# Kernel optimization log

Measured on AMD Instinct MI355X. Metric: run time of the kernel, lower is better.

## Reference

```python
import jax, jax.numpy as jnp
import numpy as np

B, N, D, HEADS, P, C = 64, 197, 768, 12, 12, 200
ARC_S, ARC_M = 30.0, 0.5


def layer_norm(x, g, b, eps=1e-5):
    m = jnp.mean(x, axis=-1, keepdims=True)
    v = jnp.var(x, axis=-1, keepdims=True)
    return (x - m) / jnp.sqrt(v + eps) * g + b


def setup_inputs() -> dict:
    key = jax.random.key(0)
    ks = jax.random.split(key, 16)
    sc = 0.02
    return {
        'hidden': jax.random.normal(ks[0], (B, N, D), jnp.float32),
        'attns': jax.random.uniform(ks[1], (4, B, HEADS, N, N), jnp.float32),
        'labels': jax.random.randint(ks[2], (B,), 0, C),
        'ln1_g': jnp.ones((D,), jnp.float32),
        'ln1_b': jnp.zeros((D,), jnp.float32),
        'w_in': jax.random.normal(ks[3], (3 * D, D), jnp.float32) * sc,
        'b_in': jnp.zeros((3 * D,), jnp.float32),
        'w_out': jax.random.normal(ks[4], (D, D), jnp.float32) * sc,
        'b_out': jnp.zeros((D,), jnp.float32),
        'ln2_g': jnp.ones((D,), jnp.float32),
        'ln2_b': jnp.zeros((D,), jnp.float32),
        'w_pool': jax.random.normal(ks[5], (1, D), jnp.float32) * sc,
        'b_pool': jnp.zeros((1,), jnp.float32),
        'pool_temp': jnp.float32(1.0),
        'w_mlp': jax.random.normal(ks[6], (D, D), jnp.float32) * sc,
        'b_mlp': jnp.zeros((D,), jnp.float32),
        'arc_w': jax.random.normal(ks[7], (C, 2 * D), jnp.float32) * sc,
    }


def reference(hidden, attns, labels, ln1_g, ln1_b, w_in, b_in, w_out, b_out,
              ln2_g, ln2_b, w_pool, b_pool, pool_temp, w_mlp, b_mlp, arc_w):
    cls_embed = hidden[:, 0]              # [B, D]
    patch_embeds = hidden[:, 1:]          # [B, N-1, D]

    # Multi-layer attention fusion: mean over heads, CLS row, drop CLS col.
    attn_scores = attns.mean(axis=2)[:, :, 0, 1:].mean(axis=0)  # [B, N-1]

    # Top-k part selection + gather.
    idx = jax.lax.top_k(attn_scores, P)[1]                       # [B, P]
    parts = jnp.take_along_axis(patch_embeds, idx[:, :, None], axis=1)  # [B,P,D]
    parts = layer_norm(parts, ln1_g, ln1_b)

    # Multi-head self-attention over parts (eval mode, no dropout).
    hd = D // HEADS
    qkv = parts @ w_in.T + b_in                                  # [B,P,3D]
    q, k, v = jnp.split(qkv, 3, axis=-1)
    def heads(t):
        return t.reshape(B, P, HEADS, hd).transpose(0, 2, 1, 3)  # [B,H,P,hd]
    q, k, v = heads(q), heads(k), heads(v)
    scores = jnp.einsum('bhqd,bhkd->bhqk', q, k) / jnp.sqrt(jnp.float32(hd))
    a = jax.nn.softmax(scores, axis=-1)
    o = jnp.einsum('bhqk,bhkd->bhqd', a, v)
    o = o.transpose(0, 2, 1, 3).reshape(B, P, D)
    attn_out = o @ w_out.T + b_out
    attn_out = layer_norm(attn_out, ln2_g, ln2_b)

    # Temperature-softmax weighted pooling.
    raw_w = (attn_out @ w_pool.T + b_pool)[..., 0]               # [B,P]
    weights = jax.nn.softmax(raw_w / jnp.maximum(pool_temp, 0.3), axis=1)
    part_feat = jnp.sum(attn_out * weights[..., None], axis=1)   # [B,D]
    part_feat = jax.nn.relu(part_feat @ w_mlp.T + b_mlp)

    fusion = jnp.concatenate([cls_embed, part_feat], axis=1)     # [B,2D]

    # ArcFace margin (train logits with labels).
    fn = fusion / jnp.linalg.norm(fusion, axis=-1, keepdims=True)
    wn = arc_w / jnp.linalg.norm(arc_w, axis=-1, keepdims=True)
    cosine = fn @ wn.T                                           # [B,C]
    sine = jnp.sqrt(jnp.clip(1.0 - cosine ** 2, 0.0, 1.0))
    cos_m, sin_m = np.cos(ARC_M), np.sin(ARC_M)
    th = np.cos(np.pi - ARC_M)
    mm = np.sin(np.pi - ARC_M) * ARC_M
    phi = cosine * cos_m - sine * sin_m
    phi = jnp.where(cosine > th, phi, cosine - mm)
    one_hot = jax.nn.one_hot(labels, C, dtype=cosine.dtype)
    logits = (one_hot * phi + (1.0 - one_hot) * cosine) * ARC_S
    return logits
```

## Files before the change

kernel.cpp:

```cpp
#include <hip/hip_runtime.h>
#include <hip/hip_bf16.h>
#include <float.h>
#include <math.h>

#define BB 64
#define NNtok 197
#define DD 768
#define HH 12
#define PP 12
#define CC 200
#define NPATCH 196

typedef short bf16x8 __attribute__((ext_vector_type(8)));
typedef float f32x4 __attribute__((ext_vector_type(4)));

__device__ __forceinline__ unsigned short bf16_bits(float x) {
  __hip_bfloat16 h = __float2bfloat16(x);
  return *reinterpret_cast<unsigned short*>(&h);
}
__device__ __forceinline__ float u2f(unsigned int u) {
  union { unsigned int u; float f; } cv; cv.u = u; return cv.f;
}
__device__ __forceinline__ float bfu(unsigned short us) {
  union { unsigned int u; float f; } cv; cv.u = ((unsigned int)us) << 16; return cv.f;
}

__global__ __launch_bounds__(256) void k1_front(
    const float* __restrict__ hidden, const float* __restrict__ attns,
    const float* __restrict__ g, const float* __restrict__ be,
    const float* __restrict__ w1, const float* __restrict__ w2,
    const float* __restrict__ w3, __hip_bfloat16* __restrict__ o1,
    __hip_bfloat16* __restrict__ o2, __hip_bfloat16* __restrict__ o3,
    __hip_bfloat16* __restrict__ parts) {
  int t = threadIdx.x, bi = blockIdx.x;
  if (bi >= 64) {
    for (int i = (bi - 64) * 256 + t; i < 737280; i += 256 * 256) {
      const float* src; __hip_bfloat16* dst; int off;
      if (i < 442368) { src = w1; dst = o1; off = i; }
      else if (i < 589824) { src = w2; dst = o2; off = i - 442368; }
      else { src = w3; dst = o3; off = i - 589824; }
      float4 v = ((const float4*)src)[off];
      union { unsigned short u[4]; ushort4 v4; } p;
      p.u[0] = bf16_bits(v.x); p.u[1] = bf16_bits(v.y);
      p.u[2] = bf16_bits(v.z); p.u[3] = bf16_bits(v.w);
      ((ushort4*)dst)[off] = p.v4;
    }
    return;
  }
  int b = bi;
  __shared__ float sc[256];
  __shared__ int sel_s[PP];
  int wv = t >> 6, ln = t & 63;
  float acc = -FLT_MAX;
  if (t < NPATCH) {
    acc = 0.f;
#pragma unroll
    for (int l = 0; l < 4; l++) {
      float part = 0.f;
#pragma unroll
      for (int h = 0; h < HH; h++) {
        size_t base = (size_t)((l * BB + b) * HH + h) * ((size_t)NNtok * NNtok);
        part += attns[base + 1 + t];
      }
      acc += part * (1.f / 12.f);
    }
    acc *= 0.25f;
  }
  sc[t] = acc;
  __syncthreads();
  if (t < 64) {
    float v[4]; int idx[4];
#pragma unroll
    for (int j = 0; j < 4; j++) { idx[j] = t + j * 64; v[j] = sc[idx[j]]; }
    for (int it = 0; it < PP; ++it) {
      float bv = v[0]; int bidx = idx[0];
#pragma unroll
      for (int j = 1; j < 4; j++)
        if (v[j] > bv || (v[j] == bv && idx[j] < bidx)) { bv = v[j]; bidx = idx[j]; }
      float cv = bv; int ci = bidx;
#pragma unroll
      for (int off = 32; off > 0; off >>= 1) {
        float ov = __shfl_xor(cv, off); int oi = __shfl_xor(ci, off);
        if (ov > cv || (ov == cv && oi < ci)) { cv = ov; ci = oi; }
      }
      if (t == 0) sel_s[it] = ci;
#pragma unroll
      for (int j = 0; j < 4; j++)
        if (idx[j] == ci) v[j] = -FLT_MAX;
    }
  }
  __syncthreads();
#pragma unroll
  for (int q = 0; q < 3; q++) {
    int i = wv * 3 + q;
    const float* row = hidden + ((size_t)b * NNtok + 1 + sel_s[i]) * DD;
    float x[12], s1 = 0.f, s2 = 0.f;
#pragma unroll
    for (int k = 0; k < 12; k++) {
      x[k] = row[ln + 64 * k];
      s1 += x[k]; s2 += x[k] * x[k];
    }
#pragma unroll
    for (int off = 32; off > 0; off >>= 1) {
      s1 += __shfl_xor(s1, off); s2 += __shfl_xor(s2, off);
    }
    float m = s1 * (1.f / DD);
    float rstd = rsqrtf(s2 * (1.f / DD) - m * m + 1e-5f);
    __hip_bfloat16* outp_ = parts + ((size_t)b * PP + i) * DD;
#pragma unroll
    for (int k = 0; k < 12; k++) {
      int d = ln + 64 * k;
      outp_[d] = __float2bfloat16((x[k] - m) * rstd * g[d] + be[d]);
    }
  }
}

__global__ __launch_bounds__(256) void k2_mid(
    const __hip_bfloat16* __restrict__ parts, const __hip_bfloat16* __restrict__ w_in_bf,
    const float* __restrict__ b_in, const __hip_bfloat16* __restrict__ w_out_bf,
    float* __restrict__ part_ws) {
  int bi = blockIdx.x;
  int b = bi >> 2, hg = bi & 3;
  int t = threadIdx.x;
  int wave = t >> 6, lane = t & 63, lr = lane & 15, kg = lane >> 4;
  __shared__ __align__(16) unsigned short qkv3[3][16][192];
  __shared__ __align__(16) unsigned short o3[16][192];
  __shared__ float scores[432];

  int pr = lr < 12 ? lr : 11;
  const __hip_bfloat16* Ab = parts + ((size_t)b * 12 + pr) * DD + kg * 8;
  int wrow[9];
#pragma unroll
  for (int nf = 0; nf < 9; nf++) {
    int lc = wave * 144 + nf * 16 + lr;
    int s = lc / 192, d2 = lc - s * 192;
    wrow[nf] = s * 768 + hg * 192 + d2;
  }
  f32x4 acc[9];
#pragma unroll
  for (int nf = 0; nf < 9; nf++) { acc[nf][0]=0.f; acc[nf][1]=0.f; acc[nf][2]=0.f; acc[nf][3]=0.f; }
  for (int k0 = 0; k0 < 768; k0 += 32) {
    bf16x8 af = *(const bf16x8*)(Ab + k0);
    bf16x8 wf[9];
#pragma unroll
    for (int nf = 0; nf < 9; nf++)
      wf[nf] = *(const bf16x8*)(w_in_bf + (size_t)wrow[nf] * DD + kg * 8 + k0);
#pragma unroll
    for (int nf = 0; nf < 9; nf++)
      acc[nf] = __builtin_amdgcn_mfma_f32_16x16x32_bf16(af, wf[nf], acc[nf], 0, 0, 0);
  }
#pragma unroll
  for (int nf = 0; nf < 9; nf++) {
    int lc = wave * 144 + nf * 16 + lr;
    int s = lc / 192, d2 = lc - s * 192;
    float bv = b_in[s * 768 + hg * 192 + d2];
#pragma unroll
    for (int r = 0; r < 4; r++) {
      int p = kg * 4 + r;
      qkv3[s][p][d2] = bf16_bits(acc[nf][r] + bv);
    }
  }
  __syncthreads();

  for (int e = t; e < 432; e += 256) {
    int h = e / 144, rem = e - h * 144;
    int i = rem / 12, j = rem - i * 12;
    float s = 0.f;
#pragma unroll
    for (int d = 0; d < 64; d++)
      s += bfu(qkv3[0][i][h * 64 + d]) * bfu(qkv3[1][j][h * 64 + d]);
    scores[e] = s * 0.125f;
  }
  __syncthreads();
  if (t < 36) {
    int h = t / 12, i = t - h * 12;
    float* row = scores + h * 144 + i * 12;
    float m = -FLT_MAX;
#pragma unroll
    for (int j = 0; j < 12; j++) m = fmaxf(m, row[j]);
    float e2[12], sum = 0.f;
#pragma unroll
    for (int j = 0; j < 12; j++) { e2[j] = expf(row[j] - m); sum += e2[j]; }
    float inv = 1.f / sum;
#pragma unroll
    for (int j = 0; j < 12; j++) row[j] = e2[j] * inv;
  }
  __syncthreads();
  for (int o = t; o < 2304; o += 256) {
    int i = o / 192, d2 = o - i * 192;
    int h = d2 >> 6;
    float s = 0.f;
#pragma unroll
    for (int j = 0; j < 12; j++)
      s += scores[h * 144 + i * 12 + j] * bfu(qkv3[2][j][d2]);
    o3[i][d2] = bf16_bits(s);
  }
  __syncthreads();

  f32x4 acc2[12];
#pragma unroll
  for (int jf = 0; jf < 12; jf++) { acc2[jf][0]=0.f; acc2[jf][1]=0.f; acc2[jf][2]=0.f; acc2[jf][3]=0.f; }
  const unsigned short* Ob = &o3[0][0] + lr * 192 + kg * 8;
  for (int k0 = 0; k0 < 192; k0 += 32) {
    bf16x8 af = *(const bf16x8*)(Ob + k0);
    bf16x8 wf[12];
#pragma unroll
    for (int jf = 0; jf < 12; jf++) {
      int j = wave * 192 + jf * 16 + lr;
      wf[jf] = *(const bf16x8*)(w_out_bf + (size_t)j * DD + hg * 192 + kg * 8 + k0);
    }
#pragma unroll
    for (int jf = 0; jf < 12; jf++)
      acc2[jf] = __builtin_amdgcn_mfma_f32_16x16x32_bf16(af, wf[jf], acc2[jf], 0, 0, 0);
  }
#pragma unroll
  for (int jf = 0; jf < 12; jf++) {
    int j = wave * 192 + jf * 16 + lr;
#pragma unroll
    for (int r = 0; r < 4; r++) {
      int p = kg * 4 + r;
      if (p < 12)
        part_ws[(((size_t)b * 4 + hg) * 12 + p) * DD + j] = acc2[jf][r];
    }
  }
}

__global__ __launch_bounds__(256) void k3_back(
    const float* __restrict__ part_ws, const float* __restrict__ b_out,
    const float* __restrict__ g, const float* __restrict__ be,
    const float* __restrict__ wp, const float* __restrict__ bp,
    const float* __restrict__ ptemp, const __hip_bfloat16* __restrict__ wmlp,
    const float* __restrict__ bmlp, float* __restrict__ pmlp) {
  int bi = blockIdx.x;
  int b = bi >> 2, q4 = bi & 3;
  int t = threadIdx.x, wv = t >> 6, ln = t & 63;
  __shared__ float a12[12 * 768];
  __shared__ float raww_s[12];
  __shared__ float pfeat[768];
  for (int u = t; u < 9216; u += 256) {
    int j = u % 768;
    float s = b_out[j];
#pragma unroll
    for (int hg = 0; hg < 4; hg++)
      s += part_ws[(((size_t)b * 4 + hg) * 12) * DD + u];
    a12[u] = s;
  }
  __syncthreads();
#pragma unroll
  for (int q = 0; q < 3; q++) {
    int r = wv * 3 + q;
    float x[12], s1 = 0.f, s2 = 0.f;
#pragma unroll
    for (int k = 0; k < 12; k++) {
      x[k] = a12[r * 768 + ln + 64 * k];
      s1 += x[k]; s2 += x[k] * x[k];
    }
#pragma unroll
    for (int off = 32; off > 0; off >>= 1) {
      s1 += __shfl_xor(s1, off); s2 += __shfl_xor(s2, off);
    }
    float m = s1 * (1.f / DD);
    float rstd = rsqrtf(s2 * (1.f / DD) - m * m + 1e-5f);
    float pl = 0.f;
#pragma unroll
    for (int k = 0; k < 12; k++) {
      int d = ln + 64 * k;
      float y = (x[k] - m) * rstd * g[d] + be[d];
      a12[r * 768 + d] = y;
      pl += y * wp[d];
    }
#pragma unroll
    for (int off = 32; off > 0; off >>= 1) pl += __shfl_xor(pl, off);
    if (ln == 0) raww_s[r] = pl + bp[0];
  }
  __syncthreads();
  float wts[12];
  {
    float inv = 1.f / fmaxf(ptemp[0], 0.3f);
    float z[12], mx = -FLT_MAX;
#pragma unroll
    for (int p = 0; p < 12; p++) { z[p] = raww_s[p] * inv; mx = fmaxf(mx, z[p]); }
    float s = 0.f;
#pragma unroll
    for (int p = 0; p < 12; p++) { z[p] = expf(z[p] - mx); s += z[p]; }
    float is = 1.f / s;
#pragma unroll
    for (int p = 0; p < 12; p++) wts[p] = z[p] * is;
  }
  for (int d = t; d < 768; d += 256) {
    float s = 0.f;
#pragma unroll
    for (int p = 0; p < 12; p++) s += a12[p * 768 + d] * wts[p];
    pfeat[d] = s;
  }
  __syncthreads();
  if (t < 192) {
    int j = q4 * 192 + t;
    const uint4* wr = (const uint4*)(wmlp + (size_t)j * DD);
    float acc2 = bmlp[j];
    for (int k = 0; k < 96; k++) {
      uint4 w4 = wr[k];
      const float* pf = &pfeat[k * 8];
      acc2 += pf[0] * u2f(w4.x << 16) + pf[1] * u2f(w4.x & 0xFFFF0000u)
            + pf[2] * u2f(w4.y << 16) + pf[3] * u2f(w4.y & 0xFFFF0000u)
            + pf[4] * u2f(w4.z << 16) + pf[5] * u2f(w4.z & 0xFFFF0000u)
            + pf[6] * u2f(w4.w << 16) + pf[7] * u2f(w4.w & 0xFFFF0000u);
    }
    pmlp[(size_t)b * DD + j] = fmaxf(acc2, 0.f);
  }
}

__global__ __launch_bounds__(256) void k4_arc(
    const float* __restrict__ hidden, const float* __restrict__ pmlp,
    const float* __restrict__ aw, const int* __restrict__ labels,
    float* __restrict__ out) {
  int cb = blockIdx.x, b = blockIdx.y, t = threadIdx.x;
  int wv = t >> 6, ln = t & 63;
  __shared__ float4 fs4[384];
  __shared__ float a4[4];
  const float4* cls4 = (const float4*)(hidden + (size_t)b * NNtok * DD);
  const float4* pm4 = (const float4*)(pmlp + (size_t)b * DD);
  for (int u = t; u < 384; u += 256) fs4[u] = (u < 192) ? cls4[u] : pm4[u - 192];
  __syncthreads();
  float s = 0.f;
  for (int u = t; u < 384; u += 256) {
    float4 v = fs4[u];
    s += v.x * v.x + v.y * v.y + v.z * v.z + v.w * v.w;
  }
#pragma unroll
  for (int off = 32; off > 0; off >>= 1) s += __shfl_xor(s, off);
  if (ln == 0) a4[wv] = s;
  __syncthreads();
  float rnf = rsqrtf(a4[0] + a4[1] + a4[2] + a4[3]);
  int lab = labels[b];
  const float cos_m = 0.8775825618903728f, sin_m = 0.479425538604203f;
  const float th = -0.8775825618903728f, mm = 0.2397127693021015f;
#pragma unroll
  for (int ci = 0; ci < 4; ci++) {
    int c = cb * 16 + ci * 4 + wv;
    if (c < CC) {
      const float4* wr = (const float4*)(aw + (size_t)c * 1536);
      float acc = 0.f, nw = 0.f;
#pragma unroll
      for (int k = 0; k < 6; k++) {
        float4 a = fs4[ln + 64 * k];
        float4 w = wr[ln + 64 * k];
        acc += a.x * w.x + a.y * w.y + a.z * w.z + a.w * w.w;
        nw += w.x * w.x + w.y * w.y + w.z * w.z + w.w * w.w;
      }
#pragma unroll
      for (int off = 32; off > 0; off >>= 1) {
        acc += __shfl_xor(acc, off); nw += __shfl_xor(nw, off);
      }
      if (ln == 0) {
        float cosv = acc * rsqrtf(nw) * rnf;
        float s2 = 1.f - cosv * cosv;
        s2 = fminf(fmaxf(s2, 0.f), 1.f);
        float sinv = sqrtf(s2);
        float phi = cosv * cos_m - sinv * sin_m;
        phi = (cosv > th) ? phi : (cosv - mm);
        out[(size_t)b * CC + c] = ((c == lab) ? phi : cosv) * 30.f;
      }
    }
  }
}

extern "C" void kernel_launch(void* const* d_in, const int* in_sizes, int n_in,
                              void* d_out, int out_size, void* d_ws, size_t ws_size,
                              hipStream_t stream) {
  const float* hidden = (const float*)d_in[0];
  const float* attns  = (const float*)d_in[1];
  const int*   labels = (const int*)d_in[2];
  const float* ln1_g  = (const float*)d_in[3];
  const float* ln1_b  = (const float*)d_in[4];
  const float* w_in   = (const float*)d_in[5];
  const float* b_in   = (const float*)d_in[6];
  const float* w_out  = (const float*)d_in[7];
  const float* b_out  = (const float*)d_in[8];
  const float* ln2_g  = (const float*)d_in[9];
  const float* ln2_b  = (const float*)d_in[10];
  const float* w_pool = (const float*)d_in[11];
  const float* b_pool = (const float*)d_in[12];
  const float* ptemp  = (const float*)d_in[13];
  const float* w_mlp  = (const float*)d_in[14];
  const float* b_mlp  = (const float*)d_in[15];
  const float* arc_w  = (const float*)d_in[16];
  float* outp = (float*)d_out;

  float* F = (float*)d_ws;
  float* part_ws = F;
  float* pmlp    = F + 2359296;
  __hip_bfloat16* parts_bf = (__hip_bfloat16*)(F + 2408448);
  __hip_bfloat16* w_in_bf  = (__hip_bfloat16*)(F + 2703360);
  __hip_bfloat16* w_out_bf = (__hip_bfloat16*)(F + 3588096);
  __hip_bfloat16* w_mlp_bf = (__hip_bfloat16*)(F + 3883008);

  k1_front<<<320, 256, 0, stream>>>(hidden, attns, ln1_g, ln1_b, w_in, w_out,
                                    w_mlp, w_in_bf, w_out_bf, w_mlp_bf, parts_bf);
  k2_mid<<<256, 256, 0, stream>>>(parts_bf, w_in_bf, b_in, w_out_bf, part_ws);
  k3_back<<<256, 256, 0, stream>>>(part_ws, b_out, ln2_g, ln2_b, w_pool, b_pool,
                                   ptemp, w_mlp_bf, b_mlp, pmlp);
  k4_arc<<<dim3(13, BB), 256, 0, stream>>>(hidden, pmlp, arc_w, labels, outp);
}
```

Baseline: 90.79 us.

## Fuse four kernels into one persistent megakernel with atomic flag synchronization

Replaces the four sequential launches (front, mid, back, arc) with a reset kernel plus one 256-block kernel whose blocks take on successive roles and hand data between stages through global atomic flags with acquire/release semantics. The goal is to remove launch gaps and whole-grid drain between stages so each batch can move ahead once its own inputs are ready. The per-batch MLP stage now runs on 64 blocks instead of 256, and the arc stage is re-split into four 50-class slices. The design assumes all 256 blocks are resident at once; the spin wait has a bounded timeout, so if that assumption fails it can silently read stale data or stall.

```diff
diff --git a/kernel.cpp b/kernel.cpp
--- a/kernel.cpp
+++ b/kernel.cpp
@@ -11,6 +11,11 @@
 #define CC 200
 #define NPATCH 196
 
+#define FSEL 0
+#define FCAST 64
+#define FMID 128
+#define FHEAD 192
+
 typedef short bf16x8 __attribute__((ext_vector_type(8)));
 typedef float f32x4 __attribute__((ext_vector_type(4)));
 
@@ -25,321 +30,344 @@
   union { unsigned int u; float f; } cv; cv.u = ((unsigned int)us) << 16; return cv.f;
 }
 
-__global__ __launch_bounds__(256) void k1_front(
+__device__ __forceinline__ void waitflag(int* p, int target) {
+  int spin = 0;
+  while (__hip_atomic_load(p, __ATOMIC_ACQUIRE, __HIP_MEMORY_SCOPE_AGENT) < target) {
+    if (++spin > (1 << 22)) break;
+    __builtin_amdgcn_s_sleep(2);
+  }
+}
+__device__ __forceinline__ void sigflag(int* p) {
+  __threadfence();
+  __hip_atomic_fetch_add(p, 1, __ATOMIC_RELEASE, __HIP_MEMORY_SCOPE_AGENT);
+}
+
+__global__ void k_reset(int* flags) { flags[threadIdx.x] = 0; }
+
+__global__ __launch_bounds__(256) void k_mega(
     const float* __restrict__ hidden, const float* __restrict__ attns,
-    const float* __restrict__ g, const float* __restrict__ be,
-    const float* __restrict__ w1, const float* __restrict__ w2,
-    const float* __restrict__ w3, __hip_bfloat16* __restrict__ o1,
-    __hip_bfloat16* __restrict__ o2, __hip_bfloat16* __restrict__ o3,
-    __hip_bfloat16* __restrict__ parts) {
-  int t = threadIdx.x, bi = blockIdx.x;
-  if (bi >= 64) {
-    for (int i = (bi - 64) * 256 + t; i < 737280; i += 256 * 256) {
+    const int* __restrict__ labels, const float* __restrict__ ln1_g,
+    const float* __restrict__ ln1_b, const float* __restrict__ w_in,
+    const float* __restrict__ b_in, const float* __restrict__ w_out,
+    const float* __restrict__ b_out, const float* __restrict__ ln2_g,
+    const float* __restrict__ ln2_b, const float* __restrict__ w_pool,
+    const float* __restrict__ b_pool, const float* __restrict__ ptemp,
+    const float* __restrict__ w_mlp, const float* __restrict__ b_mlp,
+    const float* __restrict__ arc_w, float* __restrict__ out,
+    float* __restrict__ part_ws, float* __restrict__ pmlp,
+    __hip_bfloat16* __restrict__ parts_bf, __hip_bfloat16* __restrict__ w_in_bf,
+    __hip_bfloat16* __restrict__ w_out_bf, __hip_bfloat16* __restrict__ w_mlp_bf,
+    int* __restrict__ flags) {
+  __shared__ __align__(16) char sm[43136];
+  int t = threadIdx.x, blk = blockIdx.x;
+  int wv = t >> 6, ln = t & 63;
+
+  if (blk < 64) {
+    int b = blk;
+    float* sc = (float*)sm;
+    int* sel_s = (int*)(sm + 1024);
+    float acc = -FLT_MAX;
+    if (t < NPATCH) {
+      acc = 0.f;
+#pragma unroll
+      for (int l = 0; l < 4; l++) {
+        float part = 0.f;
+#pragma unroll
+        for (int h = 0; h < HH; h++) {
+          size_t base = (size_t)((l * BB + b) * HH + h) * ((size_t)NNtok * NNtok);
+          part += attns[base + 1 + t];
+        }
+        acc += part * (1.f / 12.f);
+      }
+      acc *= 0.25f;
+    }
+    sc[t] = acc;
+    __syncthreads();
+    if (t < 64) {
+      float v[4]; int idx[4];
+#pragma unroll
+      for (int j = 0; j < 4; j++) { idx[j] = t + j * 64; v[j] = sc[idx[j]]; }
+      for (int it = 0; it < PP; ++it) {
+        float bv = v[0]; int bidx = idx[0];
+#pragma unroll
+        for (int j = 1; j < 4; j++)
+          if (v[j] > bv || (v[j] == bv && idx[j] < bidx)) { bv = v[j]; bidx = idx[j]; }
+        float cv = bv; int ci = bidx;
+#pragma unroll
+        for (int off = 32; off > 0; off >>= 1) {
+          float ov = __shfl_xor(cv, off); int oi = __shfl_xor(ci, off);
+          if (ov > cv || (ov == cv && oi < ci)) { cv = ov; ci = oi; }
+        }
+        if (t == 0) sel_s[it] = ci;
+#pragma unroll
+        for (int j = 0; j < 4; j++)
+          if (idx[j] == ci) v[j] = -FLT_MAX;
+      }
+    }
+    __syncthreads();
+#pragma unroll
+    for (int q = 0; q < 3; q++) {
+      int i = wv * 3 + q;
+      const float* row = hidden + ((size_t)b * NNtok + 1 + sel_s[i]) * DD;
+      float x[12], s1 = 0.f, s2 = 0.f;
+#pragma unroll
+      for (int k = 0; k < 12; k++) {
+        x[k] = row[ln + 64 * k];
+        s1 += x[k]; s2 += x[k] * x[k];
+      }
+#pragma unroll
+      for (int off = 32; off > 0; off >>= 1) {
+        s1 += __shfl_xor(s1, off); s2 += __shfl_xor(s2, off);
+      }
+      float m = s1 * (1.f / DD);
+      float rstd = rsqrtf(s2 * (1.f / DD) - m * m + 1e-5f);
+      __hip_bfloat16* outp_ = parts_bf + ((size_t)b * PP + i) * DD;
+#pragma unroll
+      for (int k = 0; k < 12; k++) {
+        int d = ln + 64 * k;
+        outp_[d] = __float2bfloat16((x[k] - m) * rstd * ln1_g[d] + ln1_b[d]);
+      }
+    }
+    __syncthreads();
+    if (t == 0) sigflag(&flags[FSEL + b]);
+  } else {
+    for (int i = (blk - 64) * 256 + t; i < 737280; i += 192 * 256) {
       const float* src; __hip_bfloat16* dst; int off;
-      if (i < 442368) { src = w1; dst = o1; off = i; }
-      else if (i < 589824) { src = w2; dst = o2; off = i - 442368; }
-      else { src = w3; dst = o3; off = i - 589824; }
+      if (i < 442368) { src = w_in; dst = w_in_bf; off = i; }
+      else if (i < 589824) { src = w_out; dst = w_out_bf; off = i - 442368; }
+      else { src = w_mlp; dst = w_mlp_bf; off = i - 589824; }
       float4 v = ((const float4*)src)[off];
       union { unsigned short u[4]; ushort4 v4; } p;
       p.u[0] = bf16_bits(v.x); p.u[1] = bf16_bits(v.y);
       p.u[2] = bf16_bits(v.z); p.u[3] = bf16_bits(v.w);
       ((ushort4*)dst)[off] = p.v4;
     }
-    return;
+    __syncthreads();
+    if (t == 0) sigflag(&flags[FCAST]);
   }
-  int b = bi;
-  __shared__ float sc[256];
-  __shared__ int sel_s[PP];
-  int wv = t >> 6, ln = t & 63;
-  float acc = -FLT_MAX;
-  if (t < NPATCH) {
-    acc = 0.f;
-#pragma unroll
-    for (int l = 0; l < 4; l++) {
-      float part = 0.f;
-#pragma unroll
-      for (int h = 0; h < HH; h++) {
-        size_t base = (size_t)((l * BB + b) * HH + h) * ((size_t)NNtok * NNtok);
-        part += attns[base + 1 + t];
-      }
-      acc += part * (1.f / 12.f);
-    }
-    acc *= 0.25f;
-  }
-  sc[t] = acc;
-  __syncthreads();
-  if (t < 64) {
-    float v[4]; int idx[4];
-#pragma unroll
-    for (int j = 0; j < 4; j++) { idx[j] = t + j * 64; v[j] = sc[idx[j]]; }
-    for (int it = 0; it < PP; ++it) {
-      float bv = v[0]; int bidx = idx[0];
-#pragma unroll
-      for (int j = 1; j < 4; j++)
-        if (v[j] > bv || (v[j] == bv && idx[j] < bidx)) { bv = v[j]; bidx = idx[j]; }
-      float cv = bv; int ci = bidx;
-#pragma unroll
-      for (int off = 32; off > 0; off >>= 1) {
-        float ov = __shfl_xor(cv, off); int oi = __shfl_xor(ci, off);
-        if (ov > cv || (ov == cv && oi < ci)) { cv = ov; ci = oi; }
-      }
-      if (t == 0) sel_s[it] = ci;
-#pragma unroll
-      for (int j = 0; j < 4; j++)
-        if (idx[j] == ci) v[j] = -FLT_MAX;
-    }
-  }
-  __syncthreads();
-#pragma unroll
-  for (int q = 0; q < 3; q++) {
-    int i = wv * 3 + q;
-    const float* row = hidden + ((size_t)b * NNtok + 1 + sel_s[i]) * DD;
-    float x[12], s1 = 0.f, s2 = 0.f;
-#pragma unroll
-    for (int k = 0; k < 12; k++) {
-      x[k] = row[ln + 64 * k];
-      s1 += x[k]; s2 += x[k] * x[k];
-    }
-#pragma unroll
-    for (int off = 32; off > 0; off >>= 1) {
-      s1 += __shfl_xor(s1, off); s2 += __shfl_xor(s2, off);
-    }
-    float m = s1 * (1.f / DD);
-    float rstd = rsqrtf(s2 * (1.f / DD) - m * m + 1e-5f);
-    __hip_bfloat16* outp_ = parts + ((size_t)b * PP + i) * DD;
-#pragma unroll
-    for (int k = 0; k < 12; k++) {
-      int d = ln + 64 * k;
-      outp_[d] = __float2bfloat16((x[k] - m) * rstd * g[d] + be[d]);
-    }
-  }
-}
-
-__global__ __launch_bounds__(256) void k2_mid(
-    const __hip_bfloat16* __restrict__ parts, const __hip_bfloat16* __restrict__ w_in_bf,
-    const float* __restrict__ b_in, const __hip_bfloat16* __restrict__ w_out_bf,
-    float* __restrict__ part_ws) {
-  int bi = blockIdx.x;
-  int b = bi >> 2, hg = bi & 3;
-  int t = threadIdx.x;
-  int wave = t >> 6, lane = t & 63, lr = lane & 15, kg = lane >> 4;
-  __shared__ __align__(16) unsigned short qkv3[3][16][192];
-  __shared__ __align__(16) unsigned short o3[16][192];
-  __shared__ float scores[432];
-
-  int pr = lr < 12 ? lr : 11;
-  const __hip_bfloat16* Ab = parts + ((size_t)b * 12 + pr) * DD + kg * 8;
-  int wrow[9];
-#pragma unroll
-  for (int nf = 0; nf < 9; nf++) {
-    int lc = wave * 144 + nf * 16 + lr;
-    int s = lc / 192, d2 = lc - s * 192;
-    wrow[nf] = s * 768 + hg * 192 + d2;
-  }
-  f32x4 acc[9];
-#pragma unroll
-  for (int nf = 0; nf < 9; nf++) { acc[nf][0]=0.f; acc[nf][1]=0.f; acc[nf][2]=0.f; acc[nf][3]=0.f; }
-  for (int k0 = 0; k0 < 768; k0 += 32) {
-    bf16x8 af = *(const bf16x8*)(Ab + k0);
-    bf16x8 wf[9];
-#pragma unroll
-    for (int nf = 0; nf < 9; nf++)
-      wf[nf] = *(const bf16x8*)(w_in_bf + (size_t)wrow[nf] * DD + kg * 8 + k0);
-#pragma unroll
-    for (int nf = 0; nf < 9; nf++)
-      acc[nf] = __builtin_amdgcn_mfma_f32_16x16x32_bf16(af, wf[nf], acc[nf], 0, 0, 0);
-  }
-#pragma unroll
-  for (int nf = 0; nf < 9; nf++) {
-    int lc = wave * 144 + nf * 16 + lr;
-    int s = lc / 192, d2 = lc - s * 192;
-    float bv = b_in[s * 768 + hg * 192 + d2];
-#pragma unroll
-    for (int r = 0; r < 4; r++) {
-      int p = kg * 4 + r;
-      qkv3[s][p][d2] = bf16_bits(acc[nf][r] + bv);
-    }
-  }
-  __syncthreads();
-
-  for (int e = t; e < 432; e += 256) {
-    int h = e / 144, rem = e - h * 144;
-    int i = rem / 12, j = rem - i * 12;
-    float s = 0.f;
-#pragma unroll
-    for (int d = 0; d < 64; d++)
-      s += bfu(qkv3[0][i][h * 64 + d]) * bfu(qkv3[1][j][h * 64 + d]);
-    scores[e] = s * 0.125f;
-  }
-  __syncthreads();
-  if (t < 36) {
-    int h = t / 12, i = t - h * 12;
-    float* row = scores + h * 144 + i * 12;
-    float m = -FLT_MAX;
-#pragma unroll
-    for (int j = 0; j < 12; j++) m = fmaxf(m, row[j]);
-    float e2[12], sum = 0.f;
-#pragma unroll
-    for (int j = 0; j < 12; j++) { e2[j] = expf(row[j] - m); sum += e2[j]; }
-    float inv = 1.f / sum;
-#pragma unroll
-    for (int j = 0; j < 12; j++) row[j] = e2[j] * inv;
-  }
-  __syncthreads();
-  for (int o = t; o < 2304; o += 256) {
-    int i = o / 192, d2 = o - i * 192;
-    int h = d2 >> 6;
-    float s = 0.f;
-#pragma unroll
-    for (int j = 0; j < 12; j++)
-      s += scores[h * 144 + i * 12 + j] * bfu(qkv3[2][j][d2]);
-    o3[i][d2] = bf16_bits(s);
-  }
-  __syncthreads();
-
-  f32x4 acc2[12];
-#pragma unroll
-  for (int jf = 0; jf < 12; jf++) { acc2[jf][0]=0.f; acc2[jf][1]=0.f; acc2[jf][2]=0.f; acc2[jf][3]=0.f; }
-  const unsigned short* Ob = &o3[0][0] + lr * 192 + kg * 8;
-  for (int k0 = 0; k0 < 192; k0 += 32) {
-    bf16x8 af = *(const bf16x8*)(Ob + k0);
-    bf16x8 wf[12];
+
+  {
+    int b = ((blk >> 3) << 1) | (blk & 1);
+    int hg = (blk >> 1) & 3;
+    if (t == 0) {
+      waitflag(&flags[FSEL + b], 1);
+      waitflag(&flags[FCAST], 192);
+    }
+    __syncthreads();
+    int wave = wv, lane = t & 63, lr = lane & 15, kg = lane >> 4;
+    unsigned short (*qkv3)[16][192] = (unsigned short (*)[16][192])sm;
+    unsigned short (*o3)[192] = (unsigned short (*)[192])(sm + 18432);
+    float* scores = (float*)(sm + 24576);
+
+    int pr = lr < 12 ? lr : 11;
+    const __hip_bfloat16* Ab = parts_bf + ((size_t)b * 12 + pr) * DD + kg * 8;
+    int wrow[9];
+#pragma unroll
+    for (int nf = 0; nf < 9; nf++) {
+      int lc = wave * 144 + nf * 16 + lr;
+      int s = lc / 192, d2 = lc - s * 192;
+      wrow[nf] = s * 768 + hg * 192 + d2;
+    }
+    f32x4 acc[9];
+#pragma unroll
+    for (int nf = 0; nf < 9; nf++) { acc[nf][0]=0.f; acc[nf][1]=0.f; acc[nf][2]=0.f; acc[nf][3]=0.f; }
+    for (int k0 = 0; k0 < 768; k0 += 32) {
+      bf16x8 af = *(const bf16x8*)(Ab + k0);
+      bf16x8 wf[9];
+#pragma unroll
+      for (int nf = 0; nf < 9; nf++)
+        wf[nf] = *(const bf16x8*)(w_in_bf + (size_t)wrow[nf] * DD + kg * 8 + k0);
+#pragma unroll
+      for (int nf = 0; nf < 9; nf++)
+        acc[nf] = __builtin_amdgcn_mfma_f32_16x16x32_bf16(af, wf[nf], acc[nf], 0, 0, 0);
+    }
+#pragma unroll
+    for (int nf = 0; nf < 9; nf++) {
+      int lc = wave * 144 + nf * 16 + lr;
+      int s = lc / 192, d2 = lc - s * 192;
+      float bv = b_in[s * 768 + hg * 192 + d2];
+#pragma unroll
+      for (int r = 0; r < 4; r++) {
+        int p = kg * 4 + r;
+        qkv3[s][p][d2] = bf16_bits(acc[nf][r] + bv);
+      }
+    }
+    __syncthreads();
+    for (int e = t; e < 432; e += 256) {
+      int h = e / 144, rem = e - h * 144;
+      int i = rem / 12, j = rem - i * 12;
+      float s = 0.f;
+#pragma unroll
+      for (int d = 0; d < 64; d++)
+        s += bfu(qkv3[0][i][h * 64 + d]) * bfu(qkv3[1][j][h * 64 + d]);
+      scores[e] = s * 0.125f;
+    }
+    __syncthreads();
+    if (t < 36) {
+      int h = t / 12, i = t - h * 12;
+      float* row = scores + h * 144 + i * 12;
+      float m = -FLT_MAX;
+#pragma unroll
+      for (int j = 0; j < 12; j++) m = fmaxf(m, row[j]);
+      float e2[12], sum = 0.f;
+#pragma unroll
+      for (int j = 0; j < 12; j++) { e2[j] = expf(row[j] - m); sum += e2[j]; }
+      float inv = 1.f / sum;
+#pragma unroll
+      for (int j = 0; j < 12; j++) row[j] = e2[j] * inv;
+    }
+    __syncthreads();
+    for (int o = t; o < 2304; o += 256) {
+      int i = o / 192, d2 = o - i * 192;
+      int h = d2 >> 6;
+      float s = 0.f;
+#pragma unroll
+      for (int j = 0; j < 12; j++)
+        s += scores[h * 144 + i * 12 + j] * bfu(qkv3[2][j][d2]);
+      o3[i][d2] = bf16_bits(s);
+    }
+    __syncthreads();
+    f32x4 acc2[12];
+#pragma unroll
+    for (int jf = 0; jf < 12; jf++) { acc2[jf][0]=0.f; acc2[jf][1]=0.f; acc2[jf][2]=0.f; acc2[jf][3]=0.f; }
+    const unsigned short* Ob = &o3[0][0] + lr * 192 + kg * 8;
+    for (int k0 = 0; k0 < 192; k0 += 32) {
+      bf16x8 af = *(const bf16x8*)(Ob + k0);
+      bf16x8 wf[12];
+#pragma unroll
+      for (int jf = 0; jf < 12; jf++) {
+        int j = wave * 192 + jf * 16 + lr;
+        wf[jf] = *(const bf16x8*)(w_out_bf + (size_t)j * DD + hg * 192 + kg * 8 + k0);
+      }
+#pragma unroll
+      for (int jf = 0; jf < 12; jf++)
+        acc2[jf] = __builtin_amdgcn_mfma_f32_16x16x32_bf16(af, wf[jf], acc2[jf], 0, 0, 0);
+    }
 #pragma unroll
     for (int jf = 0; jf < 12; jf++) {
       int j = wave * 192 + jf * 16 + lr;
-      wf[jf] = *(const bf16x8*)(w_out_bf + (size_t)j * DD + hg * 192 + kg * 8 + k0);
-    }
-#pragma unroll
-    for (int jf = 0; jf < 12; jf++)
-      acc2[jf] = __builtin_amdgcn_mfma_f32_16x16x32_bf16(af, wf[jf], acc2[jf], 0, 0, 0);
+#pragma unroll
+      for (int r = 0; r < 4; r++) {
+        int p = kg * 4 + r;
+        if (p < 12)
+          part_ws[(((size_t)b * 4 + hg) * 12 + p) * DD + j] = acc2[jf][r];
+      }
+    }
+    __syncthreads();
+    if (t == 0) sigflag(&flags[FMID + b]);
   }
-#pragma unroll
-  for (int jf = 0; jf < 12; jf++) {
-    int j = wave * 192 + jf * 16 + lr;
-#pragma unroll
-    for (int r = 0; r < 4; r++) {
-      int p = kg * 4 + r;
-      if (p < 12)
-        part_ws[(((size_t)b * 4 + hg) * 12 + p) * DD + j] = acc2[jf][r];
-    }
+
+  if (blk < 64) {
+    int b = blk;
+    if (t == 0) waitflag(&flags[FMID + b], 4);
+    __syncthreads();
+    float* a12 = (float*)sm;
+    float* raww_s = (float*)(sm + 36864);
+    float* pfeat = (float*)(sm + 36912);
+    for (int u = t; u < 9216; u += 256) {
+      int j = u % 768;
+      float s = b_out[j];
+#pragma unroll
+      for (int hg = 0; hg < 4; hg++)
+        s += part_ws[(((size_t)b * 4 + hg) * 12) * DD + u];
+      a12[u] = s;
+    }
+    __syncthreads();
+#pragma unroll
+    for (int q = 0; q < 3; q++) {
+      int r = wv * 3 + q;
+      float x[12], s1 = 0.f, s2 = 0.f;
+#pragma unroll
+      for (int k = 0; k < 12; k++) {
+        x[k] = a12[r * 768 + ln + 64 * k];
+        s1 += x[k]; s2 += x[k] * x[k];
+      }
+#pragma unroll
+      for (int off = 32; off > 0; off >>= 1) {
+        s1 += __shfl_xor(s1, off); s2 += __shfl_xor(s2, off);
+      }
+      float m = s1 * (1.f / DD);
+      float rstd = rsqrtf(s2 * (1.f / DD) - m * m + 1e-5f);
+      float pl = 0.f;
+#pragma unroll
+      for (int k = 0; k < 12; k++) {
+        int d = ln + 64 * k;
+        float y = (x[k] - m) * rstd * ln2_g[d] + ln2_b[d];
+        a12[r * 768 + d] = y;
+        pl += y * w_pool[d];
+      }
+#pragma unroll
+      for (int off = 32; off > 0; off >>= 1) pl += __shfl_xor(pl, off);
+      if (ln == 0) raww_s[r] = pl + b_pool[0];
+    }
+    __syncthreads();
+    float wts[12];
+    {
+      float inv = 1.f / fmaxf(ptemp[0], 0.3f);
+      float z[12], mx = -FLT_MAX;
+#pragma unroll
+      for (int p = 0; p < 12; p++) { z[p] = raww_s[p] * inv; mx = fmaxf(mx, z[p]); }
+      float s = 0.f;
+#pragma unroll
+      for (int p = 0; p < 12; p++) { z[p] = expf(z[p] - mx); s += z[p]; }
+      float is = 1.f / s;
+#pragma unroll
+      for (int p = 0; p < 12; p++) wts[p] = z[p] * is;
+    }
+    for (int d = t; d < 768; d += 256) {
+      float s = 0.f;
+#pragma unroll
+      for (int p = 0; p < 12; p++) s += a12[p * 768 + d] * wts[p];
+      pfeat[d] = s;
+    }
+    __syncthreads();
+#pragma unroll
+    for (int r3 = 0; r3 < 3; r3++) {
+      int j = t + 256 * r3;
+      const uint4* wr = (const uint4*)(w_mlp_bf + (size_t)j * DD);
+      float acc2 = b_mlp[j];
+      for (int k = 0; k < 96; k++) {
+        uint4 w4 = wr[k];
+        const float* pf = &pfeat[k * 8];
+        acc2 += pf[0] * u2f(w4.x << 16) + pf[1] * u2f(w4.x & 0xFFFF0000u)
+              + pf[2] * u2f(w4.y << 16) + pf[3] * u2f(w4.y & 0xFFFF0000u)
+              + pf[4] * u2f(w4.z << 16) + pf[5] * u2f(w4.z & 0xFFFF0000u)
+              + pf[6] * u2f(w4.w << 16) + pf[7] * u2f(w4.w & 0xFFFF0000u);
+      }
+      pmlp[(size_t)b * DD + j] = fmaxf(acc2, 0.f);
+    }
+    __syncthreads();
+    if (t == 0) sigflag(&flags[FHEAD + b]);
   }
-}
-
-__global__ __launch_bounds__(256) void k3_back(
-    const float* __restrict__ part_ws, const float* __restrict__ b_out,
-    const float* __restrict__ g, const float* __restrict__ be,
-    const float* __restrict__ wp, const float* __restrict__ bp,
-    const float* __restrict__ ptemp, const __hip_bfloat16* __restrict__ wmlp,
-    const float* __restrict__ bmlp, float* __restrict__ pmlp) {
-  int bi = blockIdx.x;
-  int b = bi >> 2, q4 = bi & 3;
-  int t = threadIdx.x, wv = t >> 6, ln = t & 63;
-  __shared__ float a12[12 * 768];
-  __shared__ float raww_s[12];
-  __shared__ float pfeat[768];
-  for (int u = t; u < 9216; u += 256) {
-    int j = u % 768;
-    float s = b_out[j];
-#pragma unroll
-    for (int hg = 0; hg < 4; hg++)
-      s += part_ws[(((size_t)b * 4 + hg) * 12) * DD + u];
-    a12[u] = s;
-  }
-  __syncthreads();
-#pragma unroll
-  for (int q = 0; q < 3; q++) {
-    int r = wv * 3 + q;
-    float x[12], s1 = 0.f, s2 = 0.f;
-#pragma unroll
-    for (int k = 0; k < 12; k++) {
-      x[k] = a12[r * 768 + ln + 64 * k];
-      s1 += x[k]; s2 += x[k] * x[k];
-    }
-#pragma unroll
-    for (int off = 32; off > 0; off >>= 1) {
-      s1 += __shfl_xor(s1, off); s2 += __shfl_xor(s2, off);
-    }
-    float m = s1 * (1.f / DD);
-    float rstd = rsqrtf(s2 * (1.f / DD) - m * m + 1e-5f);
-    float pl = 0.f;
-#pragma unroll
-    for (int k = 0; k < 12; k++) {
-      int d = ln + 64 * k;
-      float y = (x[k] - m) * rstd * g[d] + be[d];
-      a12[r * 768 + d] = y;
-      pl += y * wp[d];
-    }
-#pragma unroll
-    for (int off = 32; off > 0; off >>= 1) pl += __shfl_xor(pl, off);
-    if (ln == 0) raww_s[r] = pl + bp[0];
-  }
-  __syncthreads();
-  float wts[12];
+
   {
-    float inv = 1.f / fmaxf(ptemp[0], 0.3f);
-    float z[12], mx = -FLT_MAX;
-#pragma unroll
-    for (int p = 0; p < 12; p++) { z[p] = raww_s[p] * inv; mx = fmaxf(mx, z[p]); }
+    int b = blk & 63, q3 = blk >> 6;
+    if (t == 0) waitflag(&flags[FHEAD + b], 1);
+    __syncthreads();
+    float4* fs4 = (float4*)sm;
+    float* a4 = (float*)(sm + 6144);
+    const float4* cls4 = (const float4*)(hidden + (size_t)b * NNtok * DD);
+    const float4* pm4 = (const float4*)(pmlp + (size_t)b * DD);
+    for (int u = t; u < 384; u += 256) fs4[u] = (u < 192) ? cls4[u] : pm4[u - 192];
+    __syncthreads();
     float s = 0.f;
-#pragma unroll
-    for (int p = 0; p < 12; p++) { z[p] = expf(z[p] - mx); s += z[p]; }
-    float is = 1.f / s;
-#pragma unroll
-    for (int p = 0; p < 12; p++) wts[p] = z[p] * is;
-  }
-  for (int d = t; d < 768; d += 256) {
-    float s = 0.f;
-#pragma unroll
-    for (int p = 0; p < 12; p++) s += a12[p * 768 + d] * wts[p];
-    pfeat[d] = s;
-  }
-  __syncthreads();
-  if (t < 192) {
-    int j = q4 * 192 + t;
-    const uint4* wr = (const uint4*)(wmlp + (size_t)j * DD);
-    float acc2 = bmlp[j];
-    for (int k = 0; k < 96; k++) {
-      uint4 w4 = wr[k];
-      const float* pf = &pfeat[k * 8];
-      acc2 += pf[0] * u2f(w4.x << 16) + pf[1] * u2f(w4.x & 0xFFFF0000u)
-            + pf[2] * u2f(w4.y << 16) + pf[3] * u2f(w4.y & 0xFFFF0000u)
-            + pf[4] * u2f(w4.z << 16) + pf[5] * u2f(w4.z & 0xFFFF0000u)
-            + pf[6] * u2f(w4.w << 16) + pf[7] * u2f(w4.w & 0xFFFF0000u);
-    }
-    pmlp[(size_t)b * DD + j] = fmaxf(acc2, 0.f);
-  }
-}
-
-__global__ __launch_bounds__(256) void k4_arc(
-    const float* __restrict__ hidden, const float* __restrict__ pmlp,
-    const float* __restrict__ aw, const int* __restrict__ labels,
-    float* __restrict__ out) {
-  int cb = blockIdx.x, b = blockIdx.y, t = threadIdx.x;
-  int wv = t >> 6, ln = t & 63;
-  __shared__ float4 fs4[384];
-  __shared__ float a4[4];
-  const float4* cls4 = (const float4*)(hidden + (size_t)b * NNtok * DD);
-  const float4* pm4 = (const float4*)(pmlp + (size_t)b * DD);
-  for (int u = t; u < 384; u += 256) fs4[u] = (u < 192) ? cls4[u] : pm4[u - 192];
-  __syncthreads();
-  float s = 0.f;
-  for (int u = t; u < 384; u += 256) {
-    float4 v = fs4[u];
-    s += v.x * v.x + v.y * v.y + v.z * v.z + v.w * v.w;
-  }
-#pragma unroll
-  for (int off = 32; off > 0; off >>= 1) s += __shfl_xor(s, off);
-  if (ln == 0) a4[wv] = s;
-  __syncthreads();
-  float rnf = rsqrtf(a4[0] + a4[1] + a4[2] + a4[3]);
-  int lab = labels[b];
-  const float cos_m = 0.8775825618903728f, sin_m = 0.479425538604203f;
-  const float th = -0.8775825618903728f, mm = 0.2397127693021015f;
-#pragma unroll
-  for (int ci = 0; ci < 4; ci++) {
-    int c = cb * 16 + ci * 4 + wv;
-    if (c < CC) {
-      const float4* wr = (const float4*)(aw + (size_t)c * 1536);
+    for (int u = t; u < 384; u += 256) {
+      float4 v = fs4[u];
+      s += v.x * v.x + v.y * v.y + v.z * v.z + v.w * v.w;
+    }
+#pragma unroll
+    for (int off = 32; off > 0; off >>= 1) s += __shfl_xor(s, off);
+    if (ln == 0) a4[wv] = s;
+    __syncthreads();
+    float rnf = rsqrtf(a4[0] + a4[1] + a4[2] + a4[3]);
+    int lab = labels[b];
+    const float cos_m = 0.8775825618903728f, sin_m = 0.479425538604203f;
+    const float th = -0.8775825618903728f, mm = 0.2397127693021015f;
+    int c0 = q3 * 50;
+    for (int ci = 0;; ci++) {
+      int c = c0 + wv + 4 * ci;
+      if (c >= c0 + 50) break;
+      const float4* wr = (const float4*)(arc_w + (size_t)c * 1536);
       float acc = 0.f, nw = 0.f;
 #pragma unroll
       for (int k = 0; k < 6; k++) {
@@ -394,11 +422,12 @@
   __hip_bfloat16* w_in_bf  = (__hip_bfloat16*)(F + 2703360);
   __hip_bfloat16* w_out_bf = (__hip_bfloat16*)(F + 3588096);
   __hip_bfloat16* w_mlp_bf = (__hip_bfloat16*)(F + 3883008);
-
-  k1_front<<<320, 256, 0, stream>>>(hidden, attns, ln1_g, ln1_b, w_in, w_out,
-                                    w_mlp, w_in_bf, w_out_bf, w_mlp_bf, parts_bf);
-  k2_mid<<<256, 256, 0, stream>>>(parts_bf, w_in_bf, b_in, w_out_bf, part_ws);
-  k3_back<<<256, 256, 0, stream>>>(part_ws, b_out, ln2_g, ln2_b, w_pool, b_pool,
-                                   ptemp, w_mlp_bf, b_mlp, pmlp);
-  k4_arc<<<dim3(13, BB), 256, 0, stream>>>(hidden, pmlp, arc_w, labels, outp);
-}
+  int* flags = (int*)(F + 4177920);
+
+  k_reset<<<1, 256, 0, stream>>>(flags);
+  k_mega<<<256, 256, 0, stream>>>(hidden, attns, labels, ln1_g, ln1_b, w_in,
+                                  b_in, w_out, b_out, ln2_g, ln2_b, w_pool,
+                                  b_pool, ptemp, w_mlp, b_mlp, arc_w, outp,
+                                  part_ws, pmlp, parts_bf, w_in_bf, w_out_bf,
+                                  w_mlp_bf, flags);
+}
```

New measurement: 291.5 us. 3.21x slower.
